# Optimization experiments

Hardware: AMD Instinct MI355X
Metric: run time of the kernel (lower is better)

Reference implementation:

```python
import jax, jax.numpy as jnp
import numpy as np

EPS = 1e-5

def _inst_norm(x):
    # mean-variance normalization per (batch, channel) over spatial dims
    mu = jnp.mean(x, axis=(2, 3), keepdims=True)
    var = jnp.var(x, axis=(2, 3), keepdims=True)
    return (x - mu) / jnp.sqrt(var + EPS)

def _conv1x1(x, w, b):
    # x: (B,C,H,W), w: (O,C), b: (O,)
    return jnp.einsum('bchw,oc->bohw', x, w) + b[None, :, None, None]

def setup_inputs() -> dict:
    key = jax.random.key(0)
    ks = jax.random.split(key, 8)
    B, C, H, W = 16, 512, 64, 64
    f_c = jax.random.normal(ks[0], (B, C, H, W), dtype=jnp.float32)
    f_s = jax.random.normal(ks[1], (B, C, H, W), dtype=jnp.float32)
    w1 = jax.random.normal(ks[2], (C, C), dtype=jnp.float32) * 0.02
    b1 = jax.random.normal(ks[3], (C,), dtype=jnp.float32) * 0.02
    w2 = jax.random.normal(ks[4], (C, C), dtype=jnp.float32) * 0.02
    b2 = jax.random.normal(ks[5], (C,), dtype=jnp.float32) * 0.02
    w3 = jax.random.normal(ks[6], (C, C), dtype=jnp.float32) * 0.02
    b3 = jax.random.normal(ks[7], (C,), dtype=jnp.float32) * 0.02
    return {"f_c": f_c, "f_s": f_s, "w1": w1, "b1": b1, "w2": w2, "b2": b2, "w3": w3, "b3": b3}

def reference(f_c, f_s, w1, b1, w2, b2, w3, b3):
    b, c, h, w = f_c.shape
    f_c_norm = _inst_norm(f_c)
    f_s_norm = _inst_norm(f_s)
    fc = _conv1x1(f_c_norm, w1, b1).reshape(b, c, h * w)  # (B,C,HW)
    gs = _conv1x1(f_s_norm, w2, b2).reshape(b, c, h * w)  # (B,C,HW)
    hs = _conv1x1(f_s, w3, b3).reshape(b, c, h * w)       # (B,C,HW)
    # channel attention map (B,C,C) — softmax-free
    attn = jnp.einsum('bcn,bdn->bcd', gs, fc)
    out = jnp.einsum('bcd,bdn->bcn', attn, hs)
    return out.reshape(b, c, h, w)
```

## Files before the change

kernel.cpp:

```cpp
#include <hip/hip_runtime.h>
#include <hip/hip_bf16.h>

typedef float f4 __attribute__((ext_vector_type(4)));
typedef __bf16 bf16x4 __attribute__((ext_vector_type(4)));
typedef __bf16 bf16x8 __attribute__((ext_vector_type(8)));

#define BATCH 16
#define CCH 512
#define HW 4096

__device__ __forceinline__ void gld_lds16(const void* g, void* l) {
    __builtin_amdgcn_global_load_lds(
        (const __attribute__((address_space(1))) unsigned int*)g,
        (__attribute__((address_space(3))) unsigned int*)l, 16, 0, 0);
}

__global__ __launch_bounds__(256) void stats_conv_kernel(
    const float* __restrict__ fc, const float* __restrict__ fs,
    __bf16* __restrict__ fcb, __bf16* __restrict__ fsb,
    float* __restrict__ rstd_c, float* __restrict__ rmu_c,
    float* __restrict__ rstd_s, float* __restrict__ rmu_s)
{
    const int row = blockIdx.x;
    const int tid = threadIdx.x;
    const f4* pc4 = (const f4*)(fc + (size_t)row * HW);
    const f4* ps4 = (const f4*)(fs + (size_t)row * HW);
    f4 av[4], bv[4];
    av[0] = pc4[2 * tid];       av[1] = pc4[2 * tid + 1];
    av[2] = pc4[2 * tid + 512]; av[3] = pc4[2 * tid + 513];
    bv[0] = ps4[2 * tid];       bv[1] = ps4[2 * tid + 1];
    bv[2] = ps4[2 * tid + 512]; bv[3] = ps4[2 * tid + 513];
    float sc = 0.f, qc = 0.f, ssum = 0.f, qs = 0.f;
    #pragma unroll
    for (int u = 0; u < 4; u++)
        #pragma unroll
        for (int t = 0; t < 4; t++) {
            sc += av[u][t];  qc = fmaf(av[u][t], av[u][t], qc);
            ssum += bv[u][t]; qs = fmaf(bv[u][t], bv[u][t], qs);
        }
    if (fcb) {
        bf16x8 o0, o1, p0, p1;
        #pragma unroll
        for (int t = 0; t < 4; t++) {
            o0[t] = (__bf16)av[0][t]; o0[4 + t] = (__bf16)av[1][t];
            o1[t] = (__bf16)av[2][t]; o1[4 + t] = (__bf16)av[3][t];
            p0[t] = (__bf16)bv[0][t]; p0[4 + t] = (__bf16)bv[1][t];
            p1[t] = (__bf16)bv[2][t]; p1[4 + t] = (__bf16)bv[3][t];
        }
        *(bf16x8*)(fcb + (size_t)row * HW + 8 * tid)         = o0;
        *(bf16x8*)(fcb + (size_t)row * HW + 8 * (256 + tid)) = o1;
        *(bf16x8*)(fsb + (size_t)row * HW + 8 * tid)         = p0;
        *(bf16x8*)(fsb + (size_t)row * HW + 8 * (256 + tid)) = p1;
    }
    for (int off = 32; off > 0; off >>= 1) {
        sc   += __shfl_down(sc,   off, 64);
        qc   += __shfl_down(qc,   off, 64);
        ssum += __shfl_down(ssum, off, 64);
        qs   += __shfl_down(qs,   off, 64);
    }
    __shared__ float red[4][4];
    if ((tid & 63) == 0) {
        int w = tid >> 6;
        red[w][0] = sc; red[w][1] = qc; red[w][2] = ssum; red[w][3] = qs;
    }
    __syncthreads();
    if (tid == 0) {
        float Sc = red[0][0] + red[1][0] + red[2][0] + red[3][0];
        float Qc = red[0][1] + red[1][1] + red[2][1] + red[3][1];
        float Ss = red[0][2] + red[1][2] + red[2][2] + red[3][2];
        float Qs = red[0][3] + red[1][3] + red[2][3] + red[3][3];
        float muc = Sc * (1.f / HW), varc = Qc * (1.f / HW) - muc * muc;
        float mus = Ss * (1.f / HW), vars = Qs * (1.f / HW) - mus * mus;
        float rc = rsqrtf(varc + 1e-5f), rs = rsqrtf(vars + 1e-5f);
        rstd_c[row] = rc; rmu_c[row] = rc * muc;
        rstd_s[row] = rs; rmu_s[row] = rs * mus;
    }
}

__global__ __launch_bounds__(256) void prep_w_kernel(
    const float* __restrict__ w1, const float* __restrict__ w2, const float* __restrict__ w3,
    __bf16* __restrict__ w1t, __bf16* __restrict__ w2b, __bf16* __restrict__ w3t)
{
    int i = blockIdx.x * 256 + threadIdx.x;
    int z = blockIdx.y;
    if (z == 0)      w2b[i] = (__bf16)w2[i];
    else if (z == 1) w3t[i] = (__bf16)w3[(i & 511) * 512 + (i >> 9)];
    else             w1t[i] = (__bf16)w1[(i & 511) * 512 + (i >> 9)];
}

__global__ __launch_bounds__(256) void u_kernel(
    const float* __restrict__ w1, const float* __restrict__ b3,
    const float* __restrict__ w3, const float* __restrict__ b1,
    float* __restrict__ u1, float* __restrict__ bw3)
{
    int d = blockIdx.x * 256 + threadIdx.x;
    const float* W = blockIdx.y == 0 ? w1 : w3;
    const float* v = blockIdx.y == 0 ? b3 : b1;
    float* o       = blockIdx.y == 0 ? u1 : bw3;
    float s = 0.f;
    for (int x = 0; x < 512; x++) s += W[x * 512 + d] * v[x];
    o[d] = s;
}

__global__ __launch_bounds__(256) void b1b3_kernel(
    const float* __restrict__ b1, const float* __restrict__ b3, float* __restrict__ o)
{
    int t = threadIdx.x;
    float s = b1[t] * b3[t] + b1[t + 256] * b3[t + 256];
    for (int off = 32; off > 0; off >>= 1) s += __shfl_down(s, off, 64);
    __shared__ float ss[4];
    if ((t & 63) == 0) ss[t >> 6] = s;
    __syncthreads();
    if (t == 0) o[0] = ss[0] + ss[1] + ss[2] + ss[3];
}

template<int NP>
__global__ __launch_bounds__(128) void gram_epi_q_kernel(
    const float* __restrict__ P0, const float* __restrict__ P1,
    const float* __restrict__ P2, const float* __restrict__ P3,
    __bf16* __restrict__ G, const float* __restrict__ u1,
    const float* __restrict__ rstd_s, const float* __restrict__ rmu_s,
    const float* __restrict__ rstd_c, const float* __restrict__ rmu_c,
    float* __restrict__ q)
{
    const int row = blockIdx.x;
    const int b = row >> 9;
    const int t = threadIdx.x;
    const int d0 = t * 4;
    const size_t flat = (size_t)row * 512 + d0;
    f4 g = *(const f4*)(P0 + flat);
    if (NP == 4) {
        g += *(const f4*)(P1 + flat);
        g += *(const f4*)(P2 + flat);
        g += *(const f4*)(P3 + flat);
    }
    const float rs = rstd_s[row], rm = rmu_s[row];
    const float* rc  = rstd_c + b * 512;
    const float* rmc = rmu_c  + b * 512;
    bf16x4 o;
    float qp = 0.f;
    #pragma unroll
    for (int k = 0; k < 4; k++) {
        float val = rs * rc[d0 + k] * g[k] - 4096.f * rm * rmc[d0 + k];
        o[k] = (__bf16)val;
        qp = fmaf((float)o[k], u1[d0 + k], qp);
    }
    *(bf16x4*)(G + flat) = o;
    for (int off = 32; off > 0; off >>= 1) qp += __shfl_down(qp, off, 64);
    __shared__ float sred[2];
    if ((t & 63) == 0) sred[t >> 6] = qp;
    __syncthreads();
    if (t == 0) q[row] = sred[0] + sred[1];
}

__global__ __launch_bounds__(256) void gram_epi_kernel(
    const float* __restrict__ Graw, __bf16* __restrict__ G,
    const float* __restrict__ rstd_s, const float* __restrict__ rmu_s,
    const float* __restrict__ rstd_c, const float* __restrict__ rmu_c)
{
    size_t i4 = (size_t)blockIdx.x * 256 + threadIdx.x;
    size_t flat = i4 * 4;
    int b  = (int)(flat >> 18);
    int c  = (int)((flat >> 9) & 511);
    int d0 = (int)(flat & 511);
    float rs = rstd_s[b * 512 + c], rm = rmu_s[b * 512 + c];
    f4 g = *(const f4*)(Graw + flat);
    bf16x4 o;
    #pragma unroll
    for (int t = 0; t < 4; t++) {
        float val = rs * rstd_c[b * 512 + d0 + t] * g[t]
                  - 4096.f * rm * rmu_c[b * 512 + d0 + t];
        o[t] = (__bf16)val;
    }
    *(bf16x4*)(G + flat) = o;
    (void)c;
}

__global__ __launch_bounds__(64) void q_kernel(
    const __bf16* __restrict__ G, const float* __restrict__ u1, float* __restrict__ q)
{
    int r = blockIdx.x;
    const __bf16* row = G + (size_t)r * 512;
    float s = 0.f;
    for (int i = threadIdx.x; i < 512; i += 64) s += (float)row[i] * u1[i];
    for (int off = 32; off > 0; off >>= 1) s += __shfl_down(s, off, 64);
    if (threadIdx.x == 0) q[r] = s;
}

__global__ __launch_bounds__(64) void v2_kernel(
    const float* __restrict__ w2, const float* __restrict__ qv,
    const float* __restrict__ b2, const float* __restrict__ b1b3,
    float* __restrict__ vv)
{
    int r = blockIdx.x, b = r >> 9, c = r & 511;
    float s = 0.f;
    for (int i = threadIdx.x; i < 512; i += 64) s += w2[c * 512 + i] * qv[b * 512 + i];
    for (int off = 32; off > 0; off >>= 1) s += __shfl_down(s, off, 64);
    if (threadIdx.x == 0) vv[r] = s + 4096.f * b1b3[0] * b2[c];
}

__global__ __launch_bounds__(256) void transpose_kernel(
    const __bf16* __restrict__ in, __bf16* __restrict__ out)
{
    __shared__ __align__(16) __bf16 t[64 * 64];
    const int b = blockIdx.z, e0 = blockIdx.y * 64, n0 = blockIdx.x * 64;
    const int tid = threadIdx.x;
    const __bf16* src = in + ((size_t)b * 512 + e0) * HW + n0;
    __bf16* dst = out + ((size_t)b * HW + n0) * 512 + e0;
    #pragma unroll
    for (int it = 0; it < 2; it++) {
        int idx = it * 256 + tid;
        int e = idx >> 3, v = idx & 7;
        *(bf16x8*)&t[e * 64 + ((v ^ (e & 7)) * 8)] =
            *(const bf16x8*)(src + (size_t)e * HW + v * 8);
    }
    __syncthreads();
    #pragma unroll
    for (int it = 0; it < 2; it++) {
        int idx = it * 256 + tid;
        int n = idx >> 3, v = idx & 7;
        bf16x8 o;
        #pragma unroll
        for (int u = 0; u < 8; u++) {
            int row = v * 8 + u;
            o[u] = t[row * 64 + (((n >> 3) ^ u) * 8) + (n & 7)];
        }
        *(bf16x8*)(dst + (size_t)n * 512 + v * 8) = o;
    }
}

template<int BM, int BN, bool D_F32, bool ATOMIC, bool PARTIAL, bool NTSTORE>
__global__ __launch_bounds__(256) void gemm_nt_lds(
    const __bf16* __restrict__ A, const __bf16* __restrict__ B, void* __restrict__ D,
    int K, int splitk, int lda, int ldb, int ldd,
    long long sA, long long sB, long long sD,
    const float* __restrict__ t1, int vt1, const float* __restrict__ t2, int vt2,
    float tscale, float* __restrict__ Dalt, long long altStride)
{
    constexpr int FM = BM / 32, FN = BN / 32;
    __shared__ __align__(16) __bf16 As[BM * 64];
    __shared__ __align__(16) __bf16 Bs[BN * 64];

    const int tid = threadIdx.x;
    const int lane = tid & 63, wid = tid >> 6;
    const int b = blockIdx.z / splitk, chunk = blockIdx.z % splitk;
    const int klen = K / splitk, k0 = chunk * klen, k1 = k0 + klen;
    const int m0 = blockIdx.y * BM, n0 = blockIdx.x * BN;
    const int l16 = lane & 15, l4 = lane >> 4;
    const int wm = (wid >> 1) * (BM / 2), wn = (wid & 1) * (BN / 2);
    const int r_in = lane >> 3, slot = lane & 7;
    const int csw = (slot ^ r_in) * 8;
    const int rsw = (l16 & 7) * 8;

    const __bf16* Ab = A + (long long)b * sA;
    const __bf16* Bb = B + (long long)b * sB;

    f4 acc[FM][FN];
    #pragma unroll
    for (int i = 0; i < FM; i++)
        #pragma unroll
        for (int j = 0; j < FN; j++) acc[i][j] = (f4){0.f, 0.f, 0.f, 0.f};

    for (int kt = k0; kt < k1; kt += 64) {
        __syncthreads();
        #pragma unroll
        for (int i = 0; i < BM / 32; i++) {
            int ch = i * 4 + wid;
            gld_lds16(Ab + (long long)(m0 + ch * 8 + r_in) * lda + kt + csw,
                      As + ch * 512);
        }
        #pragma unroll
        for (int i = 0; i < BN / 32; i++) {
            int ch = i * 4 + wid;
            gld_lds16(Bb + (long long)(n0 + ch * 8 + r_in) * ldb + kt + csw,
                      Bs + ch * 512);
        }
        __syncthreads();
        #pragma unroll
        for (int kk = 0; kk < 2; kk++) {
            bf16x8 af[FM], bfr[FN];
            #pragma unroll
            for (int i = 0; i < FM; i++)
                af[i] = *(const bf16x8*)&As[(wm + i * 16 + l16) * 64 + ((kk * 32 + l4 * 8) ^ rsw)];
            #pragma unroll
            for (int j = 0; j < FN; j++)
                bfr[j] = *(const bf16x8*)&Bs[(wn + j * 16 + l16) * 64 + ((kk * 32 + l4 * 8) ^ rsw)];
            #pragma unroll
            for (int i = 0; i < FM; i++)
                #pragma unroll
                for (int j = 0; j < FN; j++)
                    acc[i][j] = __builtin_amdgcn_mfma_f32_16x16x32_bf16(af[i], bfr[j], acc[i][j], 0, 0, 0);
        }
    }

    if (PARTIAL) {
        float* base = (chunk == 0) ? (float*)D : (Dalt + (long long)(chunk - 1) * altStride);
        base += (long long)b * sD;
        #pragma unroll
        for (int j = 0; j < FN; j++) {
            int col = n0 + wn + j * 16 + l16;
            #pragma unroll
            for (int i = 0; i < FM; i++)
                #pragma unroll
                for (int rr = 0; rr < 4; rr++) {
                    int row = m0 + wm + i * 16 + l4 * 4 + rr;
                    base[(size_t)row * ldd + col] = acc[i][j][rr];
                }
        }
        return;
    }
    char* Dbase = (char*)D + (long long)b * sD * (D_F32 ? 4 : 2);
    if (ATOMIC) {
        float* D32 = (float*)Dbase;
        #pragma unroll
        for (int j = 0; j < FN; j++) {
            int col = n0 + wn + j * 16 + l16;
            #pragma unroll
            for (int i = 0; i < FM; i++)
                #pragma unroll
                for (int rr = 0; rr < 4; rr++) {
                    int row = m0 + wm + i * 16 + l4 * 4 + rr;
                    atomicAdd(D32 + (size_t)row * ldd + col, acc[i][j][rr]);
                }
        }
        return;
    }
    const float* t1b = t1 ? t1 + (long long)b * vt1 : nullptr;
    const float* t2b = t2 ? t2 + (long long)b * vt2 : nullptr;
    #pragma unroll
    for (int j = 0; j < FN; j++) {
        int col = n0 + wn + j * 16 + l16;
        float ct = t2b ? t2b[col] : 1.f;
        #pragma unroll
        for (int i = 0; i < FM; i++) {
            #pragma unroll
            for (int rr = 0; rr < 4; rr++) {
                int row = m0 + wm + i * 16 + l4 * 4 + rr;
                float val = acc[i][j][rr];
                if (t1b) val += tscale * t1b[row] * ct;
                size_t idx = (size_t)row * ldd + col;
                if (D_F32) {
                    if (NTSTORE) __builtin_nontemporal_store(val, (float*)Dbase + idx);
                    else         ((float*)Dbase)[idx] = val;
                } else {
                    ((__bf16*)Dbase)[idx] = (__bf16)val;
                }
            }
        }
    }
}

template<int BM, int BN, bool A_F32, bool B_F32, bool B_KMAJOR, bool D_F32, bool ATOMIC>
__global__ __launch_bounds__(256) void gemm_kernel(
    const void* __restrict__ Ap, const void* __restrict__ Bp, void* __restrict__ Dp,
    int K, int splitk, int lda, int ldb, int ldd,
    long long sA, long long sB, long long sD,
    const float* __restrict__ s1, int vs1, const float* __restrict__ s2, int vs2,
    const float* __restrict__ t1, int vt1, const float* __restrict__ t2, int vt2,
    float tscale)
{
    static_assert(B_KMAJOR || BN == 128, "NN staging assumes BN=128");
    constexpr int FM = BM / 32, FN = BN / 32;
    constexpr int LSA = 40;
    constexpr int LSB = B_KMAJOR ? 40 : 36;
    __shared__ __bf16 As[BM * LSA];
    __shared__ __bf16 Bs[BN * LSB];

    const int tid = threadIdx.x;
    const int b = blockIdx.z / splitk;
    const int chunk = blockIdx.z % splitk;
    const int klen = K / splitk;
    const int k0 = chunk * klen, k1 = k0 + klen;
    const int m0 = blockIdx.y * BM, n0 = blockIdx.x * BN;
    const int lane = tid & 63, wid = tid >> 6;
    const int wm = (wid >> 1) * (BM / 2), wn = (wid & 1) * (BN / 2);
    const int l16 = lane & 15, l4 = lane >> 4;

    const char* Abase = (const char*)Ap + (long long)b * sA * (A_F32 ? 4 : 2);
    const char* Bbase = (const char*)Bp + (long long)b * sB * (B_F32 ? 4 : 2);
    char* Dbase = (char*)Dp + (long long)b * sD * (D_F32 ? 4 : 2);

    f4 acc[FM][FN];
    #pragma unroll
    for (int i = 0; i < FM; i++)
        #pragma unroll
        for (int j = 0; j < FN; j++) acc[i][j] = (f4){0.f, 0.f, 0.f, 0.f};

    for (int kt = k0; kt < k1; kt += 32) {
        __syncthreads();
        if (A_F32) {
            const float* A32 = (const float*)Abase;
            #pragma unroll
            for (int it = 0; it < BM / 32; it++) {
                int q = it * 256 + tid;
                int r = q >> 3, c = (q & 7) * 4;
                f4 v = *(const f4*)(A32 + (size_t)(m0 + r) * lda + kt + c);
                bf16x4 o;
                o[0] = (__bf16)v[0]; o[1] = (__bf16)v[1]; o[2] = (__bf16)v[2]; o[3] = (__bf16)v[3];
                *(bf16x4*)&As[r * LSA + c] = o;
            }
        } else {
            const __bf16* A16 = (const __bf16*)Abase;
            #pragma unroll
            for (int it = 0; it < BM / 64; it++) {
                int q = it * 256 + tid;
                int r = q >> 2, c = (q & 3) * 8;
                *(bf16x8*)&As[r * LSA + c] = *(const bf16x8*)(A16 + (size_t)(m0 + r) * lda + kt + c);
            }
        }
        if (B_KMAJOR) {
            if (B_F32) {
                const float* B32 = (const float*)Bbase;
                #pragma unroll
                for (int it = 0; it < BN / 32; it++) {
                    int q = it * 256 + tid;
                    int r = q >> 3, c = (q & 7) * 4;
                    f4 v = *(const f4*)(B32 + (size_t)(n0 + r) * ldb + kt + c);
                    bf16x4 o;
                    o[0] = (__bf16)v[0]; o[1] = (__bf16)v[1]; o[2] = (__bf16)v[2]; o[3] = (__bf16)v[3];
                    *(bf16x4*)&Bs[r * LSB + c] = o;
                }
            } else {
                const __bf16* B16 = (const __bf16*)Bbase;
                #pragma unroll
                for (int it = 0; it < BN / 64; it++) {
                    int q = it * 256 + tid;
                    int r = q >> 2, c = (q & 3) * 8;
                    *(bf16x8*)&Bs[r * LSB + c] = *(const bf16x8*)(B16 + (size_t)(n0 + r) * ldb + kt + c);
                }
            }
        } else {
            const int n = tid & 127;
            const int kh = (tid >> 7) * 4;
            #pragma unroll
            for (int kk = 0; kk < 32; kk += 8) {
                int k = kk + kh;
                bf16x4 o;
                if (B_F32) {
                    const float* B32 = (const float*)Bbase;
                    #pragma unroll
                    for (int t = 0; t < 4; t++)
                        o[t] = (__bf16)B32[(size_t)(kt + k + t) * ldb + n0 + n];
                } else {
                    const __bf16* B16 = (const __bf16*)Bbase;
                    #pragma unroll
                    for (int t = 0; t < 4; t++)
                        o[t] = B16[(size_t)(kt + k + t) * ldb + n0 + n];
                }
                *(bf16x4*)&Bs[n * LSB + k] = o;
            }
        }
        __syncthreads();

        bf16x8 af[FM], bfr[FN];
        #pragma unroll
        for (int i = 0; i < FM; i++)
            af[i] = *(const bf16x8*)&As[(wm + i * 16 + l16) * LSA + l4 * 8];
        #pragma unroll
        for (int j = 0; j < FN; j++) {
            if (B_KMAJOR) {
                bfr[j] = *(const bf16x8*)&Bs[(wn + j * 16 + l16) * LSB + l4 * 8];
            } else {
                const __bf16* p = &Bs[(wn + j * 16 + l16) * LSB + l4 * 8];
                bf16x4 lo = *(const bf16x4*)p;
                bf16x4 hi = *(const bf16x4*)(p + 4);
                bf16x8 r;
                r[0]=lo[0]; r[1]=lo[1]; r[2]=lo[2]; r[3]=lo[3];
                r[4]=hi[0]; r[5]=hi[1]; r[6]=hi[2]; r[7]=hi[3];
                bfr[j] = r;
            }
        }
        #pragma unroll
        for (int i = 0; i < FM; i++)
            #pragma unroll
            for (int j = 0; j < FN; j++)
                acc[i][j] = __builtin_amdgcn_mfma_f32_16x16x32_bf16(af[i], bfr[j], acc[i][j], 0, 0, 0);
    }

    if (ATOMIC) {
        float* D32 = (float*)Dbase;
        #pragma unroll
        for (int j = 0; j < FN; j++) {
            int col = n0 + wn + j * 16 + l16;
            #pragma unroll
            for (int i = 0; i < FM; i++)
                #pragma unroll
                for (int rr = 0; rr < 4; rr++) {
                    int row = m0 + wm + i * 16 + l4 * 4 + rr;
                    atomicAdd(D32 + (size_t)row * ldd + col, acc[i][j][rr]);
                }
        }
        return;
    }
    const float* s1b = s1 ? s1 + (long long)b * vs1 : nullptr;
    const float* s2b = s2 ? s2 + (long long)b * vs2 : nullptr;
    const float* t1b = t1 ? t1 + (long long)b * vt1 : nullptr;
    const float* t2b = t2 ? t2 + (long long)b * vt2 : nullptr;
    #pragma unroll
    for (int j = 0; j < FN; j++) {
        int col = n0 + wn + j * 16 + l16;
        float cs = s2b ? s2b[col] : 1.f;
        float ct = t2b ? t2b[col] : 1.f;
        #pragma unroll
        for (int i = 0; i < FM; i++) {
            #pragma unroll
            for (int rr = 0; rr < 4; rr++) {
                int row = m0 + wm + i * 16 + l4 * 4 + rr;
                float val = acc[i][j][rr];
                if (s1b) val *= s1b[row];
                val *= cs;
                if (t1b) val += tscale * t1b[row] * ct;
                size_t idx = (size_t)row * ldd + col;
                if (D_F32) ((float*)Dbase)[idx] = val;
                else       ((__bf16*)Dbase)[idx] = (__bf16)val;
            }
        }
    }
}

extern "C" void kernel_launch(void* const* d_in, const int* in_sizes, int n_in,
                              void* d_out, int out_size, void* d_ws, size_t ws_size,
                              hipStream_t stream) {
    (void)in_sizes; (void)n_in; (void)out_size;
    const float* f_c = (const float*)d_in[0];
    const float* f_s = (const float*)d_in[1];
    const float* w1  = (const float*)d_in[2];
    const float* b1  = (const float*)d_in[3];
    const float* w2  = (const float*)d_in[4];
    const float* b2  = (const float*)d_in[5];
    const float* w3  = (const float*)d_in[6];
    const float* b3  = (const float*)d_in[7];
    float* out = (float*)d_out;

    char* ws = (char*)d_ws;
    float*  rstd_c = (float*)(ws + 0);
    float*  rmu_c  = (float*)(ws + 32768);
    float*  rstd_s = (float*)(ws + 65536);
    float*  rmu_s  = (float*)(ws + 98304);
    float*  vvec   = (float*)(ws + 131072);
    float*  qvec   = (float*)(ws + 163840);
    float*  u1     = (float*)(ws + 196608);
    float*  bw3    = (float*)(ws + 198656);
    float*  b1b3p  = (float*)(ws + 200704);
    __bf16* w2b    = (__bf16*)(ws + 262144);
    __bf16* w1t    = (__bf16*)(ws + 786432);
    __bf16* w3t    = (__bf16*)(ws + 1310720);
    __bf16* w13t   = (__bf16*)(ws + 1835008);
    float*  Graw   = (float*)(ws + 2359296);
    __bf16* Pt     = (__bf16*)(ws + 2359296);
    __bf16* Mbuf   = (__bf16*)(ws + 10747904);
    __bf16* G      = (__bf16*)(ws + 19136512);
    __bf16* fcb    = (__bf16*)(ws + 27525120);
    __bf16* fst    = (__bf16*)(ws + 27525120);
    __bf16* fsb    = (__bf16*)(ws + 94633984);
    float*  slab   = (float*)(ws + 161742848);
    const bool CONV  = ws_size >= (size_t)161742848;
    const bool BIGWS = ws_size >= (size_t)161742848 + (size_t)3 * 16777216;

    const long long sBig = (long long)CCH * HW;
    const long long sSm  = (long long)CCH * CCH;
    const long long sPart = (long long)BATCH * CCH * CCH;

    stats_conv_kernel<<<dim3(BATCH * CCH), 256, 0, stream>>>(
        f_c, f_s, CONV ? fcb : nullptr, CONV ? fsb : nullptr,
        rstd_c, rmu_c, rstd_s, rmu_s);
    prep_w_kernel<<<dim3(1024, 3), 256, 0, stream>>>(w1, w2, w3, w1t, w2b, w3t);
    u_kernel<<<dim3(2, 2), 256, 0, stream>>>(w1, b3, w3, b1, u1, bw3);
    b1b3_kernel<<<1, 256, 0, stream>>>(b1, b3, b1b3p);

    if (CONV && BIGWS) {
        gemm_nt_lds<128, 128, true, false, true, false><<<dim3(4, 4, BATCH * 4), 256, 0, stream>>>(
            fsb, fcb, Graw, HW, 4, HW, HW, CCH, sBig, sBig, sSm,
            nullptr, 0, nullptr, 0, 0.f, slab, sPart);
        gram_epi_q_kernel<4><<<BATCH * CCH, 128, 0, stream>>>(
            Graw, slab, slab + sPart, slab + 2 * sPart,
            G, u1, rstd_s, rmu_s, rstd_c, rmu_c, qvec);
    } else if (CONV) {
        (void)hipMemsetAsync(Graw, 0, (size_t)16777216, stream);
        gemm_nt_lds<128, 128, true, true, false, false><<<dim3(4, 4, BATCH * 4), 256, 0, stream>>>(
            fsb, fcb, Graw, HW, 4, HW, HW, CCH, sBig, sBig, sSm,
            nullptr, 0, nullptr, 0, 0.f, nullptr, 0);
        gram_epi_q_kernel<1><<<BATCH * CCH, 128, 0, stream>>>(
            Graw, nullptr, nullptr, nullptr,
            G, u1, rstd_s, rmu_s, rstd_c, rmu_c, qvec);
    } else {
        (void)hipMemsetAsync(Graw, 0, (size_t)16777216, stream);
        gemm_kernel<128,128,true,true,true,true,true><<<dim3(4, 4, BATCH * 4), 256, 0, stream>>>(
            f_s, f_c, Graw, HW, 4, HW, HW, CCH, sBig, sBig, sSm,
            nullptr,0, nullptr,0, nullptr,0, nullptr,0, 0.f);
        gram_epi_kernel<<<4096, 256, 0, stream>>>(Graw, G, rstd_s, rmu_s, rstd_c, rmu_c);
        q_kernel<<<BATCH * CCH, 64, 0, stream>>>(G, u1, qvec);
    }

    if (CONV)
        transpose_kernel<<<dim3(64, 8, BATCH), 256, 0, stream>>>(fsb, fst);

    gemm_kernel<64,64,false,false,true,false,false><<<dim3(8, 8, 1), 256, 0, stream>>>(
        w3t, w1t, w13t, CCH, 1, CCH, CCH, CCH, 0, 0, 0,
        nullptr,0, nullptr,0, nullptr,0, nullptr,0, 0.f);
    gemm_nt_lds<64, 64, false, false, false, false><<<dim3(8, 8, BATCH), 256, 0, stream>>>(
        w13t, G, Pt, CCH, 1, CCH, CCH, CCH, 0, sSm, sSm,
        nullptr, 0, nullptr, 0, 0.f, nullptr, 0);
    gemm_nt_lds<64, 64, false, false, false, false><<<dim3(8, 8, BATCH), 256, 0, stream>>>(
        w2b, Pt, Mbuf, CCH, 1, CCH, CCH, CCH, 0, sSm, sSm,
        b2, 0, bw3, 0, 4096.f, nullptr, 0);

    v2_kernel<<<BATCH * CCH, 64, 0, stream>>>(w2, qvec, b2, b1b3p, vvec);

    if (CONV)
        gemm_nt_lds<128, 128, true, false, false, true><<<dim3(32, 4, BATCH), 256, 0, stream>>>(
            Mbuf, fst, out, CCH, 1, CCH, CCH, HW, sSm, sBig, sBig,
            vvec, CCH, nullptr, 0, 1.f, nullptr, 0);
    else
        gemm_kernel<128,128,false,true,false,true,false><<<dim3(32, 4, BATCH), 256, 0, stream>>>(
            Mbuf, f_s, out, CCH, 1, CCH, HW, HW, sSm, sBig, sBig,
            nullptr,0, nullptr,0, vvec,CCH, nullptr,0, 1.f);
}
```

Before: 573.2 us.

## Use one wave per row in stats, split-K of two for Gram, larger final tile

The stats/convert kernel now assigns one 64-lane wave per (batch,channel) row, four rows per block, so the shared-memory reduction and block barrier go away. The Gram GEMM split-K factor drops from 4 to 2, which halves the partial-sum slab traffic and the reduction work in the epilogue, at the cost of fewer blocks in flight. The final output GEMM moves to a 256x128 tile to improve operand reuse, which raises register and LDS pressure and halves the grid size.

```diff
diff --git a/kernel.cpp b/kernel.cpp
--- a/kernel.cpp
+++ b/kernel.cpp
@@ -21,56 +21,50 @@
     float* __restrict__ rstd_c, float* __restrict__ rmu_c,
     float* __restrict__ rstd_s, float* __restrict__ rmu_s)
 {
-    const int row = blockIdx.x;
-    const int tid = threadIdx.x;
+    const int row  = blockIdx.x * 4 + (threadIdx.x >> 6);
+    const int lane = threadIdx.x & 63;
     const f4* pc4 = (const f4*)(fc + (size_t)row * HW);
     const f4* ps4 = (const f4*)(fs + (size_t)row * HW);
-    f4 av[4], bv[4];
-    av[0] = pc4[2 * tid];       av[1] = pc4[2 * tid + 1];
-    av[2] = pc4[2 * tid + 512]; av[3] = pc4[2 * tid + 513];
-    bv[0] = ps4[2 * tid];       bv[1] = ps4[2 * tid + 1];
-    bv[2] = ps4[2 * tid + 512]; bv[3] = ps4[2 * tid + 513];
     float sc = 0.f, qc = 0.f, ssum = 0.f, qs = 0.f;
     #pragma unroll
-    for (int u = 0; u < 4; u++)
+    for (int j = 0; j < 4; j++) {
+        const int i0 = j * 256 + 2 * lane;
+        f4 a0 = pc4[i0],       a1 = pc4[i0 + 1];
+        f4 a2 = pc4[i0 + 128], a3 = pc4[i0 + 129];
+        f4 b0 = ps4[i0],       b1 = ps4[i0 + 1];
+        f4 b2 = ps4[i0 + 128], b3 = ps4[i0 + 129];
         #pragma unroll
         for (int t = 0; t < 4; t++) {
-            sc += av[u][t];  qc = fmaf(av[u][t], av[u][t], qc);
-            ssum += bv[u][t]; qs = fmaf(bv[u][t], bv[u][t], qs);
-        }
-    if (fcb) {
-        bf16x8 o0, o1, p0, p1;
-        #pragma unroll
-        for (int t = 0; t < 4; t++) {
-            o0[t] = (__bf16)av[0][t]; o0[4 + t] = (__bf16)av[1][t];
-            o1[t] = (__bf16)av[2][t]; o1[4 + t] = (__bf16)av[3][t];
-            p0[t] = (__bf16)bv[0][t]; p0[4 + t] = (__bf16)bv[1][t];
-            p1[t] = (__bf16)bv[2][t]; p1[4 + t] = (__bf16)bv[3][t];
-        }
-        *(bf16x8*)(fcb + (size_t)row * HW + 8 * tid)         = o0;
-        *(bf16x8*)(fcb + (size_t)row * HW + 8 * (256 + tid)) = o1;
-        *(bf16x8*)(fsb + (size_t)row * HW + 8 * tid)         = p0;
-        *(bf16x8*)(fsb + (size_t)row * HW + 8 * (256 + tid)) = p1;
-    }
+            sc += a0[t] + a1[t] + a2[t] + a3[t];
+            qc = fmaf(a0[t], a0[t], fmaf(a1[t], a1[t], fmaf(a2[t], a2[t], fmaf(a3[t], a3[t], qc))));
+            ssum += b0[t] + b1[t] + b2[t] + b3[t];
+            qs = fmaf(b0[t], b0[t], fmaf(b1[t], b1[t], fmaf(b2[t], b2[t], fmaf(b3[t], b3[t], qs))));
+        }
+        if (fcb) {
+            bf16x8 oa, ob, pa, pb;
+            #pragma unroll
+            for (int t = 0; t < 4; t++) {
+                oa[t] = (__bf16)a0[t]; oa[4 + t] = (__bf16)a1[t];
+                ob[t] = (__bf16)a2[t]; ob[4 + t] = (__bf16)a3[t];
+                pa[t] = (__bf16)b0[t]; pa[4 + t] = (__bf16)b1[t];
+                pb[t] = (__bf16)b2[t]; pb[4 + t] = (__bf16)b3[t];
+            }
+            *(bf16x8*)(fcb + (size_t)row * HW + i0 * 4)         = oa;
+            *(bf16x8*)(fcb + (size_t)row * HW + (i0 + 128) * 4) = ob;
+            *(bf16x8*)(fsb + (size_t)row * HW + i0 * 4)         = pa;
+            *(bf16x8*)(fsb + (size_t)row * HW + (i0 + 128) * 4) = pb;
+        }
+    }
+    #pragma unroll
     for (int off = 32; off > 0; off >>= 1) {
         sc   += __shfl_down(sc,   off, 64);
         qc   += __shfl_down(qc,   off, 64);
         ssum += __shfl_down(ssum, off, 64);
         qs   += __shfl_down(qs,   off, 64);
     }
-    __shared__ float red[4][4];
-    if ((tid & 63) == 0) {
-        int w = tid >> 6;
-        red[w][0] = sc; red[w][1] = qc; red[w][2] = ssum; red[w][3] = qs;
-    }
-    __syncthreads();
-    if (tid == 0) {
-        float Sc = red[0][0] + red[1][0] + red[2][0] + red[3][0];
-        float Qc = red[0][1] + red[1][1] + red[2][1] + red[3][1];
-        float Ss = red[0][2] + red[1][2] + red[2][2] + red[3][2];
-        float Qs = red[0][3] + red[1][3] + red[2][3] + red[3][3];
-        float muc = Sc * (1.f / HW), varc = Qc * (1.f / HW) - muc * muc;
-        float mus = Ss * (1.f / HW), vars = Qs * (1.f / HW) - mus * mus;
+    if (lane == 0) {
+        float muc = sc * (1.f / HW), varc = qc * (1.f / HW) - muc * muc;
+        float mus = ssum * (1.f / HW), vars = qs * (1.f / HW) - mus * mus;
         float rc = rsqrtf(varc + 1e-5f), rs = rsqrtf(vars + 1e-5f);
         rstd_c[row] = rc; rmu_c[row] = rc * muc;
         rstd_s[row] = rs; rmu_s[row] = rs * mus;
@@ -129,8 +123,8 @@
     const int d0 = t * 4;
     const size_t flat = (size_t)row * 512 + d0;
     f4 g = *(const f4*)(P0 + flat);
-    if (NP == 4) {
-        g += *(const f4*)(P1 + flat);
+    if (NP >= 2) g += *(const f4*)(P1 + flat);
+    if (NP >= 4) {
         g += *(const f4*)(P2 + flat);
         g += *(const f4*)(P3 + flat);
     }
@@ -555,13 +549,13 @@
     __bf16* fsb    = (__bf16*)(ws + 94633984);
     float*  slab   = (float*)(ws + 161742848);
     const bool CONV  = ws_size >= (size_t)161742848;
-    const bool BIGWS = ws_size >= (size_t)161742848 + (size_t)3 * 16777216;
+    const bool BIGWS = ws_size >= (size_t)161742848 + (size_t)16777216;
 
     const long long sBig = (long long)CCH * HW;
     const long long sSm  = (long long)CCH * CCH;
     const long long sPart = (long long)BATCH * CCH * CCH;
 
-    stats_conv_kernel<<<dim3(BATCH * CCH), 256, 0, stream>>>(
+    stats_conv_kernel<<<dim3(BATCH * CCH / 4), 256, 0, stream>>>(
         f_c, f_s, CONV ? fcb : nullptr, CONV ? fsb : nullptr,
         rstd_c, rmu_c, rstd_s, rmu_s);
     prep_w_kernel<<<dim3(1024, 3), 256, 0, stream>>>(w1, w2, w3, w1t, w2b, w3t);
@@ -569,11 +563,11 @@
     b1b3_kernel<<<1, 256, 0, stream>>>(b1, b3, b1b3p);
 
     if (CONV && BIGWS) {
-        gemm_nt_lds<128, 128, true, false, true, false><<<dim3(4, 4, BATCH * 4), 256, 0, stream>>>(
-            fsb, fcb, Graw, HW, 4, HW, HW, CCH, sBig, sBig, sSm,
+        gemm_nt_lds<128, 128, true, false, true, false><<<dim3(4, 4, BATCH * 2), 256, 0, stream>>>(
+            fsb, fcb, Graw, HW, 2, HW, HW, CCH, sBig, sBig, sSm,
             nullptr, 0, nullptr, 0, 0.f, slab, sPart);
-        gram_epi_q_kernel<4><<<BATCH * CCH, 128, 0, stream>>>(
-            Graw, slab, slab + sPart, slab + 2 * sPart,
+        gram_epi_q_kernel<2><<<BATCH * CCH, 128, 0, stream>>>(
+            Graw, slab, nullptr, nullptr,
             G, u1, rstd_s, rmu_s, rstd_c, rmu_c, qvec);
     } else if (CONV) {
         (void)hipMemsetAsync(Graw, 0, (size_t)16777216, stream);
@@ -608,7 +602,7 @@
     v2_kernel<<<BATCH * CCH, 64, 0, stream>>>(w2, qvec, b2, b1b3p, vvec);
 
     if (CONV)
-        gemm_nt_lds<128, 128, true, false, false, true><<<dim3(32, 4, BATCH), 256, 0, stream>>>(
+        gemm_nt_lds<256, 128, true, false, false, true><<<dim3(32, 2, BATCH), 256, 0, stream>>>(
             Mbuf, fst, out, CCH, 1, CCH, CCH, HW, sSm, sBig, sBig,
             vvec, CCH, nullptr, 0, 1.f, nullptr, 0);
     else
```

Result: slower. 617.4 us (+7.7%).
